# Performance work log

Hardware: AMD Instinct MI355X
Metric: run time of the kernel (lower is better)

The kernel has to match this reference:

```python
import jax, jax.numpy as jnp
import numpy as np

B, S, H, T = 32, 1024, 1024, 256
WINDOW = 2
ITERATIONS = 3


def setup_inputs() -> dict:
    key = jax.random.key(0)
    k1, k2, k3, k4, k5, k6 = jax.random.split(key, 6)
    token_feats = jax.random.normal(k1, (B, S, H), dtype=jnp.float32)
    unary_score = jax.random.normal(k2, (B, S, T), dtype=jnp.float32)
    lengths = jax.random.randint(k3, (B,), S // 2, S + 1)  # in [S/2, S]
    mask = (jnp.arange(S)[None, :] < lengths[:, None]).astype(jnp.float32)
    transitions = jax.random.normal(k4, (WINDOW, T, T), dtype=jnp.float32)
    start_transitions = jax.random.normal(k5, (WINDOW, T), dtype=jnp.float32)
    end_transitions = jax.random.normal(k6, (WINDOW, T), dtype=jnp.float32)
    return {
        "token_feats": token_feats,
        "unary_score": unary_score,
        "mask": mask,
        "transitions": transitions,
        "start_transitions": start_transitions,
        "end_transitions": end_transitions,
        "lengths": lengths,
    }


def reference(token_feats, unary_score, mask, transitions, start_transitions,
              end_transitions, lengths):
    # mask unary (and token_feats, as in original; token_feats is unused in
    # the plain-transitions second-order path)
    unary = unary_score * mask[..., None]        # [B,S,T]
    _ = token_feats * mask[..., None]
    q = unary
    batch_range = jnp.arange(q.shape[0])
    for _it in range(ITERATIONS):
        q = jax.nn.softmax(q, axis=-1)
        left_sum = jnp.zeros_like(q)
        right_sum = jnp.zeros_like(q)
        for j in range(1, WINDOW + 1):
            # message from left neighbor at distance j
            left_sum = left_sum.at[:, j:].add(
                jnp.einsum('nsa,ab->nsb', q[:, :-j], transitions[j - 1]))
            # message from right neighbor at distance j
            right_sum = right_sum.at[:, :-j].add(
                jnp.einsum('nsb,ab->nsa', q[:, j:], transitions[j - 1]))
            # end transitions scatter-add at position lengths - j
            right_sum = right_sum.at[batch_range, lengths - j].add(
                end_transitions[j - 1])
        msg = left_sum + right_sum
        # start transitions on first WINDOW positions (broadcast over batch)
        msg = msg.at[:, 0:WINDOW].add(start_transitions)
        q = unary + msg
        q = q * mask[..., None]
    return q
```

## Files before the change

kernel.cpp:

```cpp
#include <hip/hip_runtime.h>
#include <hip/hip_bf16.h>
#include <cstdint>


typedef __attribute__((ext_vector_type(4))) float f32x4;
typedef __attribute__((ext_vector_type(8))) short bf16x8;

__device__ __forceinline__ void load_lds16(const void* g, void* l) {
    __builtin_amdgcn_global_load_lds(
        (const __attribute__((address_space(1))) void*)g,
        (__attribute__((address_space(3))) void*)l, 16, 0, 0);
}

__global__ void prep_wct(const float* __restrict__ trans,
                         __hip_bfloat16* __restrict__ wct,
                         __hip_bfloat16* __restrict__ Pa,
                         __hip_bfloat16* __restrict__ Pb) {
    int n = blockIdx.x;
    int k = threadIdx.x;
    int r = k >> 8, kk = k & 255;
    float v;
    if (r == 0)      v = trans[kk * 256 + n];
    else if (r == 1) v = trans[65536 + kk * 256 + n];
    else if (r == 2) v = trans[n * 256 + kk];
    else             v = trans[65536 + n * 256 + kk];
    wct[n * 1024 + k] = __float2bfloat16(v);
    if (threadIdx.x < 256) {
        int g = blockIdx.x * 256 + threadIdx.x;
        __hip_bfloat16* P = (g & 32768) ? Pb : Pa;
        int rem = g & 32767;
        int b = rem >> 10, wr = (rem >> 8) & 3, col = rem & 255;
        int row = b * 1028 + ((wr < 2) ? wr : 1024 + wr);
        P[row * 256 + col] = __float2bfloat16(0.f);
    }
}

__global__ __launch_bounds__(256) void softmax0(
    const float* __restrict__ src, const int* __restrict__ lengths,
    __hip_bfloat16* __restrict__ P)
{
    int row  = blockIdx.x * 4 + (threadIdx.x >> 6);
    int lane = threadIdx.x & 63;
    int b = row >> 10, s = row & 1023;
    float mval = (s < lengths[b]) ? 1.f : 0.f;
    float4 x = *((const float4*)(src + row * 256 + lane * 4));
    x.x *= mval; x.y *= mval; x.z *= mval; x.w *= mval;
    float mx = fmaxf(fmaxf(x.x, x.y), fmaxf(x.z, x.w));
    #pragma unroll
    for (int o = 32; o; o >>= 1) mx = fmaxf(mx, __shfl_xor(mx, o));
    float e0 = __expf(x.x - mx), e1 = __expf(x.y - mx);
    float e2 = __expf(x.z - mx), e3 = __expf(x.w - mx);
    float sum = e0 + e1 + e2 + e3;
    #pragma unroll
    for (int o = 32; o; o >>= 1) sum += __shfl_xor(sum, o);
    float inv = 1.0f / sum;
    union { ushort4 u; __hip_bfloat16 h[4]; } o4;
    o4.h[0] = __float2bfloat16(e0 * inv);
    o4.h[1] = __float2bfloat16(e1 * inv);
    o4.h[2] = __float2bfloat16(e2 * inv);
    o4.h[3] = __float2bfloat16(e3 * inv);
    *((ushort4*)(P + (b * 1028 + 2 + s) * 256 + lane * 4)) = o4.u;
}

__global__ __launch_bounds__(256) void mfvi_iter(
    const __hip_bfloat16* __restrict__ Pin,
    const __hip_bfloat16* __restrict__ WcT,
    const float* __restrict__ unary,
    const int* __restrict__ lengths,
    const float* __restrict__ startT,
    const float* __restrict__ endT,
    __hip_bfloat16* __restrict__ Pout,
    float* __restrict__ qout,
    int final_iter)
{
    __shared__ __hip_bfloat16 As[64 * 64];
    __shared__ __hip_bfloat16 Bs[256 * 64];
    __shared__ float redA[256];
    __shared__ float redB[256];

    int mblk = blockIdx.x;
    int b  = mblk >> 4;
    int s0 = (mblk & 15) << 6;
    int tid = threadIdx.x;
    int lane = tid & 63, wid = tid >> 6;
    int wn = wid << 6;
    int cn = lane & 15, quad = lane >> 4;

    const __hip_bfloat16* Pbase = Pin + (size_t)b * 1028 * 256;
    int sr = tid >> 3;
    int sc = tid & 7;

    f32x4 acc[4][4] = {};

    for (int ks = 0; ks < 16; ++ks) {
        int region = ks >> 2;
        int delta = (region == 0) ? -1 : (region == 1) ? -2 : (region == 2) ? 1 : 2;
        int a0 = (ks & 3) << 6;
        int k0 = ks << 6;

        #pragma unroll
        for (int c = 0; c < 2; ++c) {
            int r = c * 32 + sr;
            int grow = 2 + s0 + r + delta;
            const __hip_bfloat16* g = Pbase + grow * 256 + a0 + ((sc ^ (r & 7)) << 3);
            load_lds16(g, (char*)As + c * 4096 + tid * 16);
        }
        #pragma unroll
        for (int c = 0; c < 8; ++c) {
            int n = c * 32 + sr;
            const __hip_bfloat16* g = WcT + n * 1024 + k0 + ((sc ^ (n & 7)) << 3);
            load_lds16(g, (char*)Bs + c * 4096 + tid * 16);
        }
        __syncthreads();

        #pragma unroll
        for (int kk = 0; kk < 2; ++kk) {
            int q = (kk << 2) + quad;
            bf16x8 af[4], bfv[4];
            #pragma unroll
            for (int i = 0; i < 4; ++i) {
                int m = (i << 4) + cn;
                af[i] = *(const bf16x8*)((char*)As + m * 128 + ((q ^ (m & 7)) << 4));
            }
            #pragma unroll
            for (int j = 0; j < 4; ++j) {
                int n = wn + (j << 4) + cn;
                bfv[j] = *(const bf16x8*)((char*)Bs + n * 128 + ((q ^ (n & 7)) << 4));
            }
            #pragma unroll
            for (int i = 0; i < 4; ++i)
                #pragma unroll
                for (int j = 0; j < 4; ++j)
                    acc[i][j] = __builtin_amdgcn_mfma_f32_16x16x32_bf16(
                        af[i], bfv[j], acc[i][j], 0, 0, 0);
        }
        __syncthreads();
    }

    int len = lengths[b];
    #pragma unroll
    for (int i = 0; i < 4; ++i) {
        #pragma unroll
        for (int j = 0; j < 4; ++j) {
            int n = wn + (j << 4) + cn;
            #pragma unroll
            for (int r = 0; r < 4; ++r) {
                int s = s0 + (i << 4) + (quad << 2) + r;
                float x = acc[i][j][r];
                if (s == 0)       x += startT[n];
                if (s == 1)       x += startT[256 + n];
                if (s == len - 1) x += endT[n];
                if (s == len - 2) x += endT[256 + n];
                long idx = ((long)((b << 10) + s)) * 256 + n;
                x += unary[idx];
                acc[i][j][r] = (s < len) ? x : 0.f;
            }
        }
    }

    if (final_iter) {
        #pragma unroll
        for (int i = 0; i < 4; ++i)
            #pragma unroll
            for (int j = 0; j < 4; ++j) {
                int n = wn + (j << 4) + cn;
                #pragma unroll
                for (int r = 0; r < 4; ++r) {
                    int s = s0 + (i << 4) + (quad << 2) + r;
                    qout[((long)((b << 10) + s)) * 256 + n] = acc[i][j][r];
                }
            }
        return;
    }

    #pragma unroll
    for (int i = 0; i < 4; ++i)
        #pragma unroll
        for (int r = 0; r < 4; ++r) {
            float m4 = fmaxf(fmaxf(acc[i][0][r], acc[i][1][r]),
                             fmaxf(acc[i][2][r], acc[i][3][r]));
            m4 = fmaxf(m4, __shfl_xor(m4, 1));
            m4 = fmaxf(m4, __shfl_xor(m4, 2));
            m4 = fmaxf(m4, __shfl_xor(m4, 4));
            m4 = fmaxf(m4, __shfl_xor(m4, 8));
            if (cn == 0) redA[(wid << 6) + (i << 4) + (quad << 2) + r] = m4;
        }
    __syncthreads();
    float M[4][4];
    #pragma unroll
    for (int i = 0; i < 4; ++i)
        #pragma unroll
        for (int r = 0; r < 4; ++r) {
            int row = (i << 4) + (quad << 2) + r;
            M[i][r] = fmaxf(fmaxf(redA[row], redA[64 + row]),
                            fmaxf(redA[128 + row], redA[192 + row]));
        }
    #pragma unroll
    for (int i = 0; i < 4; ++i)
        #pragma unroll
        for (int r = 0; r < 4; ++r) {
            float s4 = 0.f;
            #pragma unroll
            for (int j = 0; j < 4; ++j) {
                float e = __expf(acc[i][j][r] - M[i][r]);
                acc[i][j][r] = e;
                s4 += e;
            }
            s4 += __shfl_xor(s4, 1);
            s4 += __shfl_xor(s4, 2);
            s4 += __shfl_xor(s4, 4);
            s4 += __shfl_xor(s4, 8);
            if (cn == 0) redB[(wid << 6) + (i << 4) + (quad << 2) + r] = s4;
        }
    __syncthreads();
    #pragma unroll
    for (int i = 0; i < 4; ++i)
        #pragma unroll
        for (int r = 0; r < 4; ++r) {
            int row = (i << 4) + (quad << 2) + r;
            float inv = 1.0f / (redB[row] + redB[64 + row] +
                                redB[128 + row] + redB[192 + row]);
            int s = s0 + row;
            #pragma unroll
            for (int j = 0; j < 4; ++j) {
                int n = wn + (j << 4) + cn;
                Pout[((size_t)b * 1028 + 2 + s) * 256 + n] =
                    __float2bfloat16(acc[i][j][r] * inv);
            }
        }
}

extern "C" void kernel_launch(void* const* d_in, const int* in_sizes, int n_in,
                              void* d_out, int out_size, void* d_ws, size_t ws_size,
                              hipStream_t stream) {
    const float* unary  = (const float*)d_in[1];
    const float* trans  = (const float*)d_in[3];
    const float* startT = (const float*)d_in[4];
    const float* endT   = (const float*)d_in[5];
    const int*   lens   = (const int*)d_in[6];

    char* ws = (char*)d_ws;
    __hip_bfloat16* Pa  = (__hip_bfloat16*)ws;
    __hip_bfloat16* Pb  = (__hip_bfloat16*)(ws + ((size_t)32 << 20));
    __hip_bfloat16* WcT = (__hip_bfloat16*)(ws + ((size_t)64 << 20));

    prep_wct<<<dim3(256), dim3(1024), 0, stream>>>(trans, WcT, Pa, Pb);
    softmax0<<<dim3(8192), dim3(256), 0, stream>>>(unary, lens, Pa);
    mfvi_iter<<<dim3(512), dim3(256), 0, stream>>>(Pa, WcT, unary, lens, startT, endT, Pb, nullptr, 0);
    mfvi_iter<<<dim3(512), dim3(256), 0, stream>>>(Pb, WcT, unary, lens, startT, endT, Pa, nullptr, 0);
    mfvi_iter<<<dim3(512), dim3(256), 0, stream>>>(Pa, WcT, unary, lens, startT, endT, nullptr, (float*)d_out, 1);
}
```

Measured before the change: 304.0 us.

## Fuse all stages into one cooperative kernel with grid syncs and restage operands

Replaces the five separate launches with a single cooperative kernel that performs the weight transpose, guard zeroing and initial softmax, then runs three MFVI iterations separated by grid-wide syncs, with a multi-launch fallback. The tile routine is restructured so the 68-row probability slab is staged once per K-half in LDS and reused across all four neighbour offsets, while transition weights are read straight from global memory instead of staged through LDS. This targets launch overhead and redundant A-tile loads, at the cost of grid.sync overhead, uncached-in-LDS B-operand global reads, and a 2-blocks-per-CU residency requirement for the cooperative launch.

```diff
diff --git a/kernel.cpp b/kernel.cpp
--- a/kernel.cpp
+++ b/kernel.cpp
@@ -1,7 +1,10 @@
 #include <hip/hip_runtime.h>
 #include <hip/hip_bf16.h>
+#include <hip/hip_cooperative_groups.h>
 #include <cstdint>
 
+
+namespace cg = cooperative_groups;
 
 typedef __attribute__((ext_vector_type(4))) float f32x4;
 typedef __attribute__((ext_vector_type(8))) short bf16x8;
@@ -12,134 +15,69 @@
         (__attribute__((address_space(3))) void*)l, 16, 0, 0);
 }
 
-__global__ void prep_wct(const float* __restrict__ trans,
-                         __hip_bfloat16* __restrict__ wct,
-                         __hip_bfloat16* __restrict__ Pa,
-                         __hip_bfloat16* __restrict__ Pb) {
-    int n = blockIdx.x;
-    int k = threadIdx.x;
-    int r = k >> 8, kk = k & 255;
-    float v;
-    if (r == 0)      v = trans[kk * 256 + n];
-    else if (r == 1) v = trans[65536 + kk * 256 + n];
-    else if (r == 2) v = trans[n * 256 + kk];
-    else             v = trans[65536 + n * 256 + kk];
-    wct[n * 1024 + k] = __float2bfloat16(v);
-    if (threadIdx.x < 256) {
-        int g = blockIdx.x * 256 + threadIdx.x;
-        __hip_bfloat16* P = (g & 32768) ? Pb : Pa;
-        int rem = g & 32767;
-        int b = rem >> 10, wr = (rem >> 8) & 3, col = rem & 255;
-        int row = b * 1028 + ((wr < 2) ? wr : 1024 + wr);
-        P[row * 256 + col] = __float2bfloat16(0.f);
-    }
-}
-
-__global__ __launch_bounds__(256) void softmax0(
-    const float* __restrict__ src, const int* __restrict__ lengths,
-    __hip_bfloat16* __restrict__ P)
+__device__ __forceinline__ void do_tile(
+    int tile, const __hip_bfloat16* __restrict__ Pin,
+    const __hip_bfloat16* __restrict__ WcT,
+    const float* __restrict__ unary, const int* __restrict__ lengths,
+    const float* __restrict__ startT, const float* __restrict__ endT,
+    __hip_bfloat16* __restrict__ Pout, float* __restrict__ out, int final_it,
+    __hip_bfloat16* Ps, float* redA, float* redB)
 {
-    int row  = blockIdx.x * 4 + (threadIdx.x >> 6);
-    int lane = threadIdx.x & 63;
-    int b = row >> 10, s = row & 1023;
-    float mval = (s < lengths[b]) ? 1.f : 0.f;
-    float4 x = *((const float4*)(src + row * 256 + lane * 4));
-    x.x *= mval; x.y *= mval; x.z *= mval; x.w *= mval;
-    float mx = fmaxf(fmaxf(x.x, x.y), fmaxf(x.z, x.w));
-    #pragma unroll
-    for (int o = 32; o; o >>= 1) mx = fmaxf(mx, __shfl_xor(mx, o));
-    float e0 = __expf(x.x - mx), e1 = __expf(x.y - mx);
-    float e2 = __expf(x.z - mx), e3 = __expf(x.w - mx);
-    float sum = e0 + e1 + e2 + e3;
-    #pragma unroll
-    for (int o = 32; o; o >>= 1) sum += __shfl_xor(sum, o);
-    float inv = 1.0f / sum;
-    union { ushort4 u; __hip_bfloat16 h[4]; } o4;
-    o4.h[0] = __float2bfloat16(e0 * inv);
-    o4.h[1] = __float2bfloat16(e1 * inv);
-    o4.h[2] = __float2bfloat16(e2 * inv);
-    o4.h[3] = __float2bfloat16(e3 * inv);
-    *((ushort4*)(P + (b * 1028 + 2 + s) * 256 + lane * 4)) = o4.u;
-}
-
-__global__ __launch_bounds__(256) void mfvi_iter(
-    const __hip_bfloat16* __restrict__ Pin,
-    const __hip_bfloat16* __restrict__ WcT,
-    const float* __restrict__ unary,
-    const int* __restrict__ lengths,
-    const float* __restrict__ startT,
-    const float* __restrict__ endT,
-    __hip_bfloat16* __restrict__ Pout,
-    float* __restrict__ qout,
-    int final_iter)
-{
-    __shared__ __hip_bfloat16 As[64 * 64];
-    __shared__ __hip_bfloat16 Bs[256 * 64];
-    __shared__ float redA[256];
-    __shared__ float redB[256];
-
-    int mblk = blockIdx.x;
-    int b  = mblk >> 4;
-    int s0 = (mblk & 15) << 6;
     int tid = threadIdx.x;
     int lane = tid & 63, wid = tid >> 6;
-    int wn = wid << 6;
-    int cn = lane & 15, quad = lane >> 4;
-
-    const __hip_bfloat16* Pbase = Pin + (size_t)b * 1028 * 256;
-    int sr = tid >> 3;
-    int sc = tid & 7;
+    int cn = lane & 15, quad = lane >> 4, wn = wid << 6;
+    int b = tile >> 4, s0 = (tile & 15) << 6;
+    int len = lengths[b];
+    const char* Pbase = (const char*)(Pin + ((size_t)b * 1028 + s0) * 256);
 
     f32x4 acc[4][4] = {};
 
-    for (int ks = 0; ks < 16; ++ks) {
-        int region = ks >> 2;
-        int delta = (region == 0) ? -1 : (region == 1) ? -2 : (region == 2) ? 1 : 2;
-        int a0 = (ks & 3) << 6;
-        int k0 = ks << 6;
-
-        #pragma unroll
-        for (int c = 0; c < 2; ++c) {
-            int r = c * 32 + sr;
-            int grow = 2 + s0 + r + delta;
-            const __hip_bfloat16* g = Pbase + grow * 256 + a0 + ((sc ^ (r & 7)) << 3);
-            load_lds16(g, (char*)As + c * 4096 + tid * 16);
-        }
-        #pragma unroll
-        for (int c = 0; c < 8; ++c) {
-            int n = c * 32 + sr;
-            const __hip_bfloat16* g = WcT + n * 1024 + k0 + ((sc ^ (n & 7)) << 3);
-            load_lds16(g, (char*)Bs + c * 4096 + tid * 16);
+    for (int h = 0; h < 2; ++h) {
+        #pragma unroll
+        for (int t = 0; t < 5; ++t) {
+            int c = t * 256 + tid;
+            if (t < 4 || tid < 64) {
+                int row = c >> 4, ch = c & 15;
+                int gch = (ch & ~7) | ((ch ^ row) & 7);
+                load_lds16(Pbase + row * 512 + h * 256 + gch * 16,
+                           (char*)Ps + c * 16);
+            }
         }
         __syncthreads();
 
-        #pragma unroll
-        for (int kk = 0; kk < 2; ++kk) {
-            int q = (kk << 2) + quad;
-            bf16x8 af[4], bfv[4];
-            #pragma unroll
-            for (int i = 0; i < 4; ++i) {
-                int m = (i << 4) + cn;
-                af[i] = *(const bf16x8*)((char*)As + m * 128 + ((q ^ (m & 7)) << 4));
-            }
-            #pragma unroll
-            for (int j = 0; j < 4; ++j) {
-                int n = wn + (j << 4) + cn;
-                bfv[j] = *(const bf16x8*)((char*)Bs + n * 128 + ((q ^ (n & 7)) << 4));
-            }
-            #pragma unroll
-            for (int i = 0; i < 4; ++i)
+        #pragma unroll 2
+        for (int p = 0; p < 8; ++p) {
+            int region = p >> 1;
+            int delta = (region == 0) ? -1 : (region == 1) ? -2
+                      : (region == 2) ?  1 : 2;
+            const __hip_bfloat16* Bk = WcT + region * 256 + h * 128 + (p & 1) * 64;
+            #pragma unroll
+            for (int kk = 0; kk < 2; ++kk) {
+                bf16x8 af[4], bfv[4];
                 #pragma unroll
                 for (int j = 0; j < 4; ++j)
-                    acc[i][j] = __builtin_amdgcn_mfma_f32_16x16x32_bf16(
-                        af[i], bfv[j], acc[i][j], 0, 0, 0);
+                    bfv[j] = *(const bf16x8*)(
+                        Bk + (size_t)(wn + (j << 4) + cn) * 1024 + kk * 32 + quad * 8);
+                int gcb = (p & 1) * 8 + kk * 4 + quad;
+                #pragma unroll
+                for (int i = 0; i < 4; ++i) {
+                    int r = (i << 4) + cn + delta + 2;
+                    int slot = (gcb & ~7) | ((gcb ^ r) & 7);
+                    af[i] = *(const bf16x8*)((const char*)Ps + r * 256 + slot * 16);
+                }
+                #pragma unroll
+                for (int i = 0; i < 4; ++i)
+                    #pragma unroll
+                    for (int j = 0; j < 4; ++j)
+                        acc[i][j] = __builtin_amdgcn_mfma_f32_16x16x32_bf16(
+                            af[i], bfv[j], acc[i][j], 0, 0, 0);
+            }
         }
         __syncthreads();
     }
 
-    int len = lengths[b];
-    #pragma unroll
-    for (int i = 0; i < 4; ++i) {
+    #pragma unroll
+    for (int i = 0; i < 4; ++i)
         #pragma unroll
         for (int j = 0; j < 4; ++j) {
             int n = wn + (j << 4) + cn;
@@ -156,9 +94,8 @@
                 acc[i][j][r] = (s < len) ? x : 0.f;
             }
         }
-    }
-
-    if (final_iter) {
+
+    if (final_it) {
         #pragma unroll
         for (int i = 0; i < 4; ++i)
             #pragma unroll
@@ -167,7 +104,7 @@
                 #pragma unroll
                 for (int r = 0; r < 4; ++r) {
                     int s = s0 + (i << 4) + (quad << 2) + r;
-                    qout[((long)((b << 10) + s)) * 256 + n] = acc[i][j][r];
+                    out[((long)((b << 10) + s)) * 256 + n] = acc[i][j][r];
                 }
             }
         return;
@@ -230,6 +167,122 @@
         }
 }
 
+__device__ __forceinline__ void wct_one(const float* __restrict__ trans,
+                                        __hip_bfloat16* __restrict__ wct, int e) {
+    int n = e >> 10, k = e & 1023;
+    int r = k >> 8, kk = k & 255;
+    float v;
+    if (r == 0)      v = trans[kk * 256 + n];
+    else if (r == 1) v = trans[65536 + kk * 256 + n];
+    else if (r == 2) v = trans[n * 256 + kk];
+    else             v = trans[65536 + n * 256 + kk];
+    wct[n * 1024 + k] = __float2bfloat16(v);
+}
+
+__device__ __forceinline__ void guard_one(__hip_bfloat16* Pa, __hip_bfloat16* Pb, int g) {
+    __hip_bfloat16* P = (g & 32768) ? Pb : Pa;
+    int rem = g & 32767;
+    int b = rem >> 10, wr = (rem >> 8) & 3, col = rem & 255;
+    int row = b * 1028 + ((wr < 2) ? wr : 1024 + wr);
+    P[row * 256 + col] = __float2bfloat16(0.f);
+}
+
+__device__ __forceinline__ void softmax0_row(const float* __restrict__ unary,
+                                             const int* __restrict__ lengths,
+                                             __hip_bfloat16* __restrict__ Pa,
+                                             int row, int lane) {
+    int b = row >> 10, s = row & 1023;
+    float mval = (s < lengths[b]) ? 1.f : 0.f;
+    float4 x = *((const float4*)(unary + (size_t)row * 256 + lane * 4));
+    x.x *= mval; x.y *= mval; x.z *= mval; x.w *= mval;
+    float mx = fmaxf(fmaxf(x.x, x.y), fmaxf(x.z, x.w));
+    #pragma unroll
+    for (int o = 32; o; o >>= 1) mx = fmaxf(mx, __shfl_xor(mx, o));
+    float ea = __expf(x.x - mx), eb = __expf(x.y - mx);
+    float ec = __expf(x.z - mx), ed = __expf(x.w - mx);
+    float sum = ea + eb + ec + ed;
+    #pragma unroll
+    for (int o = 32; o; o >>= 1) sum += __shfl_xor(sum, o);
+    float inv = 1.0f / sum;
+    union { ushort4 u; __hip_bfloat16 h[4]; } o4;
+    o4.h[0] = __float2bfloat16(ea * inv);
+    o4.h[1] = __float2bfloat16(eb * inv);
+    o4.h[2] = __float2bfloat16(ec * inv);
+    o4.h[3] = __float2bfloat16(ed * inv);
+    *((ushort4*)(Pa + ((size_t)b * 1028 + 2 + s) * 256 + lane * 4)) = o4.u;
+}
+
+__global__ __launch_bounds__(256, 2) void mfvi_coop(
+    const float* __restrict__ unary, const float* __restrict__ trans,
+    const float* __restrict__ startT, const float* __restrict__ endT,
+    const int* __restrict__ lengths,
+    __hip_bfloat16* __restrict__ Pa, __hip_bfloat16* __restrict__ Pb,
+    __hip_bfloat16* __restrict__ WcT, float* __restrict__ out)
+{
+    cg::grid_group grid = cg::this_grid();
+    __shared__ __hip_bfloat16 Ps[68 * 128];
+    __shared__ float redA[256];
+    __shared__ float redB[256];
+
+    int tid = threadIdx.x, lane = tid & 63, wid = tid >> 6;
+    int blk = blockIdx.x;
+
+    {
+        int e0 = (blk * 256 + tid) * 2;
+        wct_one(trans, WcT, e0);
+        wct_one(trans, WcT, e0 + 1);
+        if (blk >= 256 && blk < 384) {
+            int g0 = ((blk - 256) * 256 + tid) * 2;
+            guard_one(Pa, Pb, g0);
+            guard_one(Pa, Pb, g0 + 1);
+        }
+        for (int q = 0; q < 16; ++q)
+            softmax0_row(unary, lengths, Pa, blk * 64 + wid * 16 + q, lane);
+    }
+    grid.sync();
+
+    do_tile(blk, Pa, WcT, unary, lengths, startT, endT, Pb, nullptr, 0,
+            Ps, redA, redB);
+    grid.sync();
+    do_tile(blk, Pb, WcT, unary, lengths, startT, endT, Pa, nullptr, 0,
+            Ps, redA, redB);
+    grid.sync();
+    do_tile(blk, Pa, WcT, unary, lengths, startT, endT, nullptr, out, 1,
+            Ps, redA, redB);
+}
+
+__global__ __launch_bounds__(256) void prep_softmax0(
+    const float* __restrict__ unary, const float* __restrict__ trans,
+    const int* __restrict__ lengths,
+    __hip_bfloat16* __restrict__ Pa, __hip_bfloat16* __restrict__ Pb,
+    __hip_bfloat16* __restrict__ WcT)
+{
+    int tid = threadIdx.x, lane = tid & 63, wid = tid >> 6;
+    int blk = blockIdx.x;
+    int e0 = (blk * 256 + tid) * 2;
+    wct_one(trans, WcT, e0);
+    wct_one(trans, WcT, e0 + 1);
+    int idx = blk * 256 + tid;
+    if (idx < 65536) guard_one(Pa, Pb, idx);
+    else             guard_one(Pa, Pb, idx - 65536);
+    for (int q = 0; q < 16; ++q)
+        softmax0_row(unary, lengths, Pa, blk * 64 + wid * 16 + q, lane);
+}
+
+__global__ __launch_bounds__(256, 2) void mfvi_iter_k(
+    const __hip_bfloat16* __restrict__ Pin,
+    const __hip_bfloat16* __restrict__ WcT,
+    const float* __restrict__ unary, const int* __restrict__ lengths,
+    const float* __restrict__ startT, const float* __restrict__ endT,
+    __hip_bfloat16* __restrict__ Pout, float* __restrict__ out, int final_it)
+{
+    __shared__ __hip_bfloat16 Ps[68 * 128];
+    __shared__ float redA[256];
+    __shared__ float redB[256];
+    do_tile(blockIdx.x, Pin, WcT, unary, lengths, startT, endT, Pout, out,
+            final_it, Ps, redA, redB);
+}
+
 extern "C" void kernel_launch(void* const* d_in, const int* in_sizes, int n_in,
                               void* d_out, int out_size, void* d_ws, size_t ws_size,
                               hipStream_t stream) {
@@ -243,10 +296,18 @@
     __hip_bfloat16* Pa  = (__hip_bfloat16*)ws;
     __hip_bfloat16* Pb  = (__hip_bfloat16*)(ws + ((size_t)32 << 20));
     __hip_bfloat16* WcT = (__hip_bfloat16*)(ws + ((size_t)64 << 20));
-
-    prep_wct<<<dim3(256), dim3(1024), 0, stream>>>(trans, WcT, Pa, Pb);
-    softmax0<<<dim3(8192), dim3(256), 0, stream>>>(unary, lens, Pa);
-    mfvi_iter<<<dim3(512), dim3(256), 0, stream>>>(Pa, WcT, unary, lens, startT, endT, Pb, nullptr, 0);
-    mfvi_iter<<<dim3(512), dim3(256), 0, stream>>>(Pb, WcT, unary, lens, startT, endT, Pa, nullptr, 0);
-    mfvi_iter<<<dim3(512), dim3(256), 0, stream>>>(Pa, WcT, unary, lens, startT, endT, nullptr, (float*)d_out, 1);
-}
+    float* out = (float*)d_out;
+
+    void* args[] = { (void*)&unary, (void*)&trans, (void*)&startT, (void*)&endT,
+                     (void*)&lens, (void*)&Pa, (void*)&Pb, (void*)&WcT, (void*)&out };
+    hipError_t err = hipLaunchCooperativeKernel((const void*)mfvi_coop,
+                                                dim3(512), dim3(256),
+                                                args, 0, stream);
+    if (err != hipSuccess) {
+        (void)hipGetLastError();
+        prep_softmax0<<<dim3(512), dim3(256), 0, stream>>>(unary, trans, lens, Pa, Pb, WcT);
+        mfvi_iter_k<<<dim3(512), dim3(256), 0, stream>>>(Pa, WcT, unary, lens, startT, endT, Pb, nullptr, 0);
+        mfvi_iter_k<<<dim3(512), dim3(256), 0, stream>>>(Pb, WcT, unary, lens, startT, endT, Pa, nullptr, 0);
+        mfvi_iter_k<<<dim3(512), dim3(256), 0, stream>>>(Pa, WcT, unary, lens, startT, endT, nullptr, out, 1);
+    }
+}
```

New measurement: 561.1 us. 84.6% more time.
